# Kernel tuning notes

Measured on AMD Instinct MI355X. Metric: run time of the kernel, lower is better.

Reference implementation:

```python
import jax, jax.numpy as jnp
import numpy as np
import math

B, S, D = 1, 2048, 512
H = 8
DH = D // H
WIN = 128  # window_size
EPS = 1e-5


def _layernorm(x, g, b):
    mu = jnp.mean(x, axis=-1, keepdims=True)
    var = jnp.mean((x - mu) ** 2, axis=-1, keepdims=True)
    return (x - mu) * jax.lax.rsqrt(var + EPS) * g + b


def _local_attention(q, k, v, window_size):
    # q,k,v: [B,H,S,DH]. Faithful to F.pad + unfold: zero-padded keys
    # participate in softmax with score 0 (no masking), as in the original.
    w = window_size // 2
    W = 2 * w + 1
    kp = jnp.pad(k, ((0, 0), (0, 0), (w, w), (0, 0)))
    vp = jnp.pad(v, ((0, 0), (0, 0), (w, w), (0, 0)))
    idx = jnp.arange(q.shape[2])[:, None] + jnp.arange(W)[None, :]  # [S,W]
    k_win = kp[:, :, idx]  # [B,H,S,W,DH]
    v_win = vp[:, :, idx]  # [B,H,S,W,DH]
    scores = jnp.einsum('bhsd,bhswd->bhsw', q, k_win) / math.sqrt(q.shape[-1])
    attn = jax.nn.softmax(scores, axis=-1)
    return jnp.einsum('bhsw,bhswd->bhsd', attn, v_win)


def setup_inputs() -> dict:
    key = jax.random.key(0)
    ks = jax.random.split(key, 8)
    sc = 0.02
    return {
        'x': jax.random.normal(ks[0], (B, S, D), dtype=jnp.float32),
        'w_qkv': jax.random.normal(ks[1], (D, 3 * D), dtype=jnp.float32) * sc,
        'b_qkv': jnp.zeros((3 * D,), dtype=jnp.float32),
        'w_out': jax.random.normal(ks[2], (D, D), dtype=jnp.float32) * sc,
        'b_out': jnp.zeros((D,), dtype=jnp.float32),
        'ln_g': jnp.ones((D,), dtype=jnp.float32),
        'ln_b': jnp.zeros((D,), dtype=jnp.float32),
        'w1': jax.random.normal(ks[3], (D, 4 * D), dtype=jnp.float32) * sc,
        'b1': jnp.zeros((4 * D,), dtype=jnp.float32),
        'w2': jax.random.normal(ks[4], (4 * D, D), dtype=jnp.float32) * sc,
        'b2': jnp.zeros((D,), dtype=jnp.float32),
    }


def reference(x, w_qkv, b_qkv, w_out, b_out, ln_g, ln_b, w1, b1, w2, b2):
    residual = x
    xn = _layernorm(x, ln_g, ln_b)
    qkv = xn @ w_qkv + b_qkv                       # [B,S,3D]
    qkv = qkv.reshape(B, S, 3, H, DH)
    qkv = jnp.transpose(qkv, (2, 0, 3, 1, 4))      # [3,B,H,S,DH]
    q, k, v = qkv[0], qkv[1], qkv[2]
    attn_out = _local_attention(q, k, v, WIN)       # [B,H,S,DH]
    attn_out = jnp.transpose(attn_out, (0, 2, 1, 3)).reshape(B, S, D)
    attn_out = attn_out @ w_out + b_out
    out = residual + attn_out
    # FFN applied directly to `out` (no second norm in original)
    ffn = jax.nn.gelu(out @ w1 + b1, approximate=False) @ w2 + b2
    return out + ffn
```

## Files before the change

kernel.cpp:

```cpp
#include <hip/hip_runtime.h>
#include <math.h>

#define S_LEN 2048
#define DMODEL 512
#define NHEAD 8
#define DHEAD 64
#define LN_EPS 1e-5f

typedef __bf16 bf16;
typedef __bf16 bf16x8 __attribute__((ext_vector_type(8)));
typedef __bf16 bf16x4 __attribute__((ext_vector_type(4)));
typedef __bf16 bf16x2 __attribute__((ext_vector_type(2)));
typedef float f32x4 __attribute__((ext_vector_type(4)));

__device__ __forceinline__ float wave_reduce_sum(float x) {
#pragma unroll
  for (int off = 32; off > 0; off >>= 1) x += __shfl_xor(x, off);
  return x;
}

__global__ __launch_bounds__(256) void prep_kernel(
    const float* __restrict__ x, const float* __restrict__ ln_g,
    const float* __restrict__ ln_b, const float* __restrict__ w_qkv,
    const float* __restrict__ w_out, const float* __restrict__ w1,
    const float* __restrict__ w2, bf16* __restrict__ xn,
    bf16* __restrict__ wqkvT, bf16* __restrict__ woutT,
    bf16* __restrict__ w1T, bf16* __restrict__ w2T) {
  __shared__ float t[32][33];
  int b = blockIdx.x;
  const int tid = threadIdx.x;
  if (b < 2048) {
    const float2 v = ((const float2*)(x + (size_t)b * DMODEL))[tid];
    float s = v.x + v.y;
    float s2 = v.x * v.x + v.y * v.y;
    s = wave_reduce_sum(s);
    s2 = wave_reduce_sum(s2);
    __shared__ float red[2][4];
    const int wv = tid >> 6, ln = tid & 63;
    if (ln == 0) { red[0][wv] = s; red[1][wv] = s2; }
    __syncthreads();
    s = red[0][0] + red[0][1] + red[0][2] + red[0][3];
    s2 = red[1][0] + red[1][1] + red[1][2] + red[1][3];
    const float mu = s * (1.0f / DMODEL);
    const float var = s2 * (1.0f / DMODEL) - mu * mu;
    const float rs = rsqrtf(var + LN_EPS);
    const float2 gg = ((const float2*)ln_g)[tid];
    const float2 bb = ((const float2*)ln_b)[tid];
    bf16x2 o;
    o[0] = (bf16)((v.x - mu) * rs * gg.x + bb.x);
    o[1] = (bf16)((v.y - mu) * rs * gg.y + bb.y);
    ((bf16x2*)(xn + (size_t)b * DMODEL))[tid] = o;
    return;
  }
  b -= 2048;
  const float* W; bf16* WT; int K, N, bx, by;
  if (b < 768)       { W = w_qkv; WT = wqkvT; K = 512;  N = 1536; bx = b % 48; by = b / 48; }
  else if (b < 1024) { b -= 768;  W = w_out; WT = woutT; K = 512;  N = 512;  bx = b % 16; by = b / 16; }
  else if (b < 2048) { b -= 1024; W = w1;    WT = w1T;   K = 512;  N = 2048; bx = b % 64; by = b / 64; }
  else               { b -= 2048; W = w2;    WT = w2T;   K = 2048; N = 512;  bx = b % 16; by = b / 16; }
  const int c = tid & 31, r8 = tid >> 5;
  const int n0 = bx * 32, k0 = by * 32;
#pragma unroll
  for (int it = 0; it < 4; it++) {
    const int r = r8 + it * 8;
    t[r][c] = W[(size_t)(k0 + r) * N + n0 + c];
  }
  __syncthreads();
#pragma unroll
  for (int it = 0; it < 4; it++) {
    const int r = r8 + it * 8;
    WT[(size_t)(n0 + r) * K + k0 + c] = (bf16)t[c][r];
  }
}

template <int MODE, int SPLITK>
__global__ __launch_bounds__(256) void mmC_kernel(const bf16* __restrict__ A,
                                                  const bf16* __restrict__ BT,
                                                  const float* __restrict__ bias,
                                                  bf16* __restrict__ Cb,
                                                  bf16* __restrict__ vT,
                                                  float* __restrict__ outF,
                                                  int N, int K, int gx) {
  __shared__ bf16 As[2][64 * 64];
  __shared__ bf16 Bs[2][64 * 64];
  const int tid = threadIdx.x;
  int b = blockIdx.x;
  int kh = 0;
  if (SPLITK > 0) { kh = b & 1; b >>= 1; }
  const int wave = tid >> 6, lane = tid & 63;
  const int lr = lane & 15, kg = lane >> 4;
  const int wm = wave & 1, wn = wave >> 1;
  const int rowBase = (b / gx) * 64, colBase = (b % gx) * 64;
  const int ldk = (SPLITK > 0) ? 2 * SPLITK : K;
  const int kBase = kh * ((SPLITK > 0) ? SPLITK : 0);

  const bf16* aP[2]; const bf16* bP[2]; int off[2];
#pragma unroll
  for (int r = 0; r < 2; ++r) {
    const int c = wave * 2 + r;
    const int elem = c * 512 + lane * 8;
    const int s = elem >> 11, row = (elem >> 5) & 63, kp = elem & 31;
    aP[r] = A + (size_t)(rowBase + row) * ldk + kBase + s * 32 + kp;
    bP[r] = BT + (size_t)(colBase + row) * ldk + kBase + s * 32 + kp;
    off[r] = c * 512;
  }
  auto stage = [&](int kk, int buf) {
#pragma unroll
    for (int r = 0; r < 2; ++r) {
      __builtin_amdgcn_global_load_lds(
          (const __attribute__((address_space(1))) void*)(aP[r] + kk),
          (__attribute__((address_space(3))) void*)(&As[buf][off[r]]), 16, 0, 0);
      __builtin_amdgcn_global_load_lds(
          (const __attribute__((address_space(1))) void*)(bP[r] + kk),
          (__attribute__((address_space(3))) void*)(&Bs[buf][off[r]]), 16, 0, 0);
    }
  };

  f32x4 acc[2][2] = {};
  const int niter = K >> 6;
  stage(0, 0);
  for (int it = 0; it < niter; ++it) {
    const int cur = it & 1;
    __syncthreads();
    if (it + 1 < niter) stage((it + 1) << 6, cur ^ 1);
    const bf16* as = As[cur];
    const bf16* bs = Bs[cur];
#pragma unroll
    for (int s = 0; s < 2; ++s) {
      bf16x8 af[2], bfr[2];
#pragma unroll
      for (int i = 0; i < 2; ++i)
        af[i] = *(const bf16x8*)(as + s * 2048 + (wm * 32 + i * 16 + lr) * 32 + kg * 8);
#pragma unroll
      for (int j = 0; j < 2; ++j)
        bfr[j] = *(const bf16x8*)(bs + s * 2048 + (wn * 32 + j * 16 + lr) * 32 + kg * 8);
#pragma unroll
      for (int i = 0; i < 2; ++i)
#pragma unroll
        for (int j = 0; j < 2; ++j)
          acc[i][j] = __builtin_amdgcn_mfma_f32_16x16x32_bf16(af[i], bfr[j],
                                                              acc[i][j], 0, 0, 0);
    }
  }

  if (SPLITK > 0) {
#pragma unroll
    for (int j = 0; j < 2; ++j) {
      const int col = colBase + wn * 32 + j * 16 + lr;
      const float bs = (kh == 0) ? bias[col] : 0.0f;
#pragma unroll
      for (int i = 0; i < 2; ++i)
#pragma unroll
        for (int r = 0; r < 4; ++r) {
          const size_t row = rowBase + wm * 32 + i * 16 + kg * 4 + r;
          unsafeAtomicAdd(&outF[row * N + col], acc[i][j][r] + bs);
        }
    }
    return;
  }

  if (MODE == 4 && colBase >= 1024) {
#pragma unroll
    for (int j = 0; j < 2; ++j) {
      const int col = colBase + wn * 32 + j * 16 + lr;
      const float bs = bias[col];
      bf16* dst = vT + (size_t)(col - 1024) * S_LEN;
#pragma unroll
      for (int i = 0; i < 2; ++i) {
        bf16x4 p;
#pragma unroll
        for (int r = 0; r < 4; ++r) p[r] = (bf16)(acc[i][j][r] + bs);
        *(bf16x4*)(dst + rowBase + wm * 32 + i * 16 + kg * 4) = p;
      }
    }
    return;
  }

  __syncthreads();
  bf16* Cs = (bf16*)As;
#pragma unroll
  for (int j = 0; j < 2; ++j) {
    const int colL = wn * 32 + j * 16 + lr;
    const float bs = bias[colBase + colL];
#pragma unroll
    for (int i = 0; i < 2; ++i)
#pragma unroll
      for (int r = 0; r < 4; ++r) {
        const int rowL = wm * 32 + i * 16 + kg * 4 + r;
        float v = acc[i][j][r] + bs;
        if (MODE == 2) v = 0.5f * v * (1.0f + erff(v * 0.70710678118654752f));
        Cs[rowL * 64 + colL] = (bf16)v;
      }
  }
  __syncthreads();
  {
    const int rowOut = tid >> 2, colOut = (tid & 3) * 16;
    const bf16x8 v0 = *(const bf16x8*)&Cs[rowOut * 64 + colOut];
    const bf16x8 v1 = *(const bf16x8*)&Cs[rowOut * 64 + colOut + 8];
    bf16* dst = Cb + (size_t)(rowBase + rowOut) * N + colBase + colOut;
    *(bf16x8*)dst = v0;
    *(bf16x8*)(dst + 8) = v1;
  }
}

__global__ __launch_bounds__(256) void mmB_kernel(const bf16* __restrict__ A,
                                                  const bf16* __restrict__ BT,
                                                  const float* __restrict__ bias,
                                                  const float* __restrict__ res,
                                                  float* __restrict__ Cf,
                                                  bf16* __restrict__ Cb,
                                                  int N, int K) {
  __shared__ bf16 As[2][32 * 64];
  __shared__ bf16 Bs[2][64 * 64];
  const int tid = threadIdx.x;
  const int wave = tid >> 6, lane = tid & 63;
  const int lr = lane & 15, kg = lane >> 4;
  const int rowBase = blockIdx.y * 32, colBase = blockIdx.x * 64;

  const bf16* aP; const bf16* bP[2]; int aOff, bOff[2];
  {
    const int elem = wave * 512 + lane * 8;
    const int s = elem >> 10, row = (elem >> 5) & 31, kp = elem & 31;
    aP = A + (size_t)(rowBase + row) * K + s * 32 + kp;
    aOff = wave * 512;
  }
#pragma unroll
  for (int r = 0; r < 2; ++r) {
    const int c = wave * 2 + r;
    const int elem = c * 512 + lane * 8;
    const int s = elem >> 11, row = (elem >> 5) & 63, kp = elem & 31;
    bP[r] = BT + (size_t)(colBase + row) * K + s * 32 + kp;
    bOff[r] = c * 512;
  }
  auto stage = [&](int kk, int buf) {
    __builtin_amdgcn_global_load_lds(
        (const __attribute__((address_space(1))) void*)(aP + kk),
        (__attribute__((address_space(3))) void*)(&As[buf][aOff]), 16, 0, 0);
#pragma unroll
    for (int r = 0; r < 2; ++r)
      __builtin_amdgcn_global_load_lds(
          (const __attribute__((address_space(1))) void*)(bP[r] + kk),
          (__attribute__((address_space(3))) void*)(&Bs[buf][bOff[r]]), 16, 0, 0);
  };

  f32x4 acc[2] = {};
  const int niter = K >> 6;
  stage(0, 0);
  for (int it = 0; it < niter; ++it) {
    const int cur = it & 1;
    __syncthreads();
    if (it + 1 < niter) stage((it + 1) << 6, cur ^ 1);
    const bf16* as = As[cur];
    const bf16* bs = Bs[cur];
#pragma unroll
    for (int s = 0; s < 2; ++s) {
      bf16x8 af[2], bfr;
#pragma unroll
      for (int i = 0; i < 2; ++i)
        af[i] = *(const bf16x8*)(as + s * 1024 + (i * 16 + lr) * 32 + kg * 8);
      bfr = *(const bf16x8*)(bs + s * 2048 + (wave * 16 + lr) * 32 + kg * 8);
#pragma unroll
      for (int i = 0; i < 2; ++i)
        acc[i] = __builtin_amdgcn_mfma_f32_16x16x32_bf16(af[i], bfr, acc[i], 0, 0, 0);
    }
  }

  {
    const int col = colBase + wave * 16 + lr;
    const float bs = bias[col];
#pragma unroll
    for (int i = 0; i < 2; ++i)
#pragma unroll
      for (int r = 0; r < 4; ++r) {
        const size_t row = rowBase + i * 16 + kg * 4 + r;
        const float v = acc[i][r] + bs + res[row * N + col];
        Cf[row * N + col] = v;
        Cb[row * N + col] = (bf16)v;
      }
  }
}

__global__ __launch_bounds__(256) void attn_fused(const bf16* __restrict__ qkvb,
                                                  const bf16* __restrict__ vT,
                                                  bf16* __restrict__ attnb) {
  __shared__ bf16 Kl[192][72];
  __shared__ bf16 Vt[64][200];
  __shared__ bf16 Ql[64][72];

  const int tid = threadIdx.x;
  const int s0 = blockIdx.x * 64;
  const int hc = blockIdx.y * DHEAD;

  {
    const int row = tid >> 2, c0 = (tid & 3) * 16;
    const bf16* src = qkvb + (size_t)(s0 + row) * 1536 + hc + c0;
    *(bf16x8*)&Ql[row][c0] = *(const bf16x8*)src;
    *(bf16x8*)&Ql[row][c0 + 8] = *(const bf16x8*)(src + 8);
  }
#pragma unroll
  for (int it = 0; it < 3; it++) {
    const int row = it * 64 + (tid >> 2), c0 = (tid & 3) * 16;
    const int p = s0 - 64 + row;
    bf16x8 a, b;
    if (p >= 0 && p < S_LEN) {
      const bf16* src = qkvb + (size_t)p * 1536 + 512 + hc + c0;
      a = *(const bf16x8*)src;
      b = *(const bf16x8*)(src + 8);
    } else {
#pragma unroll
      for (int j = 0; j < 8; j++) { a[j] = (bf16)0.f; b[j] = (bf16)0.f; }
    }
    *(bf16x8*)&Kl[row][c0] = a;
    *(bf16x8*)&Kl[row][c0 + 8] = b;
  }
  {
    const int d = tid >> 2, r0 = (tid & 3) * 48;
    const bf16* src = vT + (size_t)(hc + d) * S_LEN;
#pragma unroll
    for (int i = 0; i < 6; i++) {
      const int p0 = s0 - 64 + r0 + i * 8;
      bf16x8 v;
      if (p0 >= 0 && p0 + 8 <= S_LEN) {
        v = *(const bf16x8*)(src + p0);
      } else {
#pragma unroll
        for (int j = 0; j < 8; j++) {
          const int p = p0 + j;
          v[j] = (p >= 0 && p < S_LEN) ? src[p] : (bf16)0.f;
        }
      }
      *(bf16x8*)&Vt[d][r0 + i * 8] = v;
    }
  }
  __syncthreads();

  const int wv = tid >> 6, lane = tid & 63;
  const int lr = lane & 15, kg = lane >> 4;

  f32x4 c[12] = {};
#pragma unroll
  for (int step = 0; step < 2; step++) {
    const bf16x8 qf = *(const bf16x8*)&Ql[wv * 16 + lr][step * 32 + kg * 8];
#pragma unroll
    for (int t = 0; t < 12; t++) {
      const bf16x8 kf = *(const bf16x8*)&Kl[t * 16 + lr][step * 32 + kg * 8];
      c[t] = __builtin_amdgcn_mfma_f32_16x16x32_bf16(qf, kf, c[t], 0, 0, 0);
    }
  }

  float e[12][4];
  float inv[4];
#pragma unroll
  for (int rr = 0; rr < 4; rr++) {
    const int q = wv * 16 + kg * 4 + rr;
    float m = -1e30f;
#pragma unroll
    for (int t = 0; t < 12; t++) {
      const int col = t * 16 + lr;
      if (col >= q && col <= q + 128) m = fmaxf(m, c[t][rr] * 0.125f);
    }
#pragma unroll
    for (int off = 1; off < 16; off <<= 1) m = fmaxf(m, __shfl_xor(m, off));
    float sum = 0.f;
#pragma unroll
    for (int t = 0; t < 12; t++) {
      const int col = t * 16 + lr;
      const bool valid = (col >= q) && (col <= q + 128);
      const float ev = valid ? __expf(c[t][rr] * 0.125f - m) : 0.f;
      e[t][rr] = ev;
      sum += ev;
    }
#pragma unroll
    for (int off = 1; off < 16; off <<= 1) sum += __shfl_xor(sum, off);
    inv[rr] = 1.f / sum;
  }

  __syncthreads();

  bf16* Pl = (bf16*)Kl + wv * (16 * 200);
#pragma unroll
  for (int rr = 0; rr < 4; rr++)
#pragma unroll
    for (int t = 0; t < 12; t++)
      Pl[(kg * 4 + rr) * 200 + t * 16 + lr] = (bf16)(e[t][rr] * inv[rr]);

  f32x4 o[4] = {};
#pragma unroll
  for (int step = 0; step < 6; step++) {
    const bf16x8 pf = *(const bf16x8*)&Pl[lr * 200 + step * 32 + kg * 8];
#pragma unroll
    for (int jt = 0; jt < 4; jt++) {
      const bf16x8 vf = *(const bf16x8*)&Vt[jt * 16 + lr][step * 32 + kg * 8];
      o[jt] = __builtin_amdgcn_mfma_f32_16x16x32_bf16(pf, vf, o[jt], 0, 0, 0);
    }
  }

#pragma unroll
  for (int jt = 0; jt < 4; jt++)
#pragma unroll
    for (int rr = 0; rr < 4; rr++) {
      const int q = wv * 16 + kg * 4 + rr;
      attnb[(size_t)(s0 + q) * DMODEL + hc + jt * 16 + lr] = (bf16)o[jt][rr];
    }
}

extern "C" void kernel_launch(void* const* d_in, const int* in_sizes, int n_in,
                              void* d_out, int out_size, void* d_ws, size_t ws_size,
                              hipStream_t stream) {
  const float* x     = (const float*)d_in[0];
  const float* w_qkv = (const float*)d_in[1];
  const float* b_qkv = (const float*)d_in[2];
  const float* w_out = (const float*)d_in[3];
  const float* b_out = (const float*)d_in[4];
  const float* ln_g  = (const float*)d_in[5];
  const float* ln_b  = (const float*)d_in[6];
  const float* w1    = (const float*)d_in[7];
  const float* b1    = (const float*)d_in[8];
  const float* w2    = (const float*)d_in[9];
  const float* b2    = (const float*)d_in[10];
  float* out = (float*)d_out;

  char* w = (char*)d_ws;
  const size_t MB = 1u << 20;
  bf16* xn    = (bf16*)(w + 0);
  bf16* attnb = (bf16*)(w + 0);
  bf16* qkvb  = (bf16*)(w + 2 * MB);
  bf16* outb  = (bf16*)(w + 2 * MB);
  bf16* vT    = (bf16*)(w + 8 * MB);
  bf16* h1    = (bf16*)(w + 10 * MB);
  bf16* wqkvT = (bf16*)(w + 18 * MB);
  bf16* woutT = (bf16*)(w + 19 * MB + 512 * 1024);
  bf16* w1T   = (bf16*)(w + 20 * MB);
  bf16* w2T   = (bf16*)(w + 22 * MB);

  prep_kernel<<<5120, 256, 0, stream>>>(x, ln_g, ln_b, w_qkv, w_out, w1, w2,
                                        xn, wqkvT, woutT, w1T, w2T);
  mmC_kernel<4, 0><<<768, 256, 0, stream>>>(xn, wqkvT, b_qkv, qkvb, vT,
                                            nullptr, 1536, 512, 24);
  attn_fused<<<dim3(32, 8), 256, 0, stream>>>(qkvb, vT, attnb);
  mmB_kernel<<<dim3(8, 64), 256, 0, stream>>>(attnb, woutT, b_out, x, out,
                                              outb, 512, 512);
  mmC_kernel<2, 0><<<1024, 256, 0, stream>>>(outb, w1T, b1, h1, nullptr,
                                             nullptr, 2048, 512, 32);
  mmC_kernel<2, 1024><<<512, 256, 0, stream>>>(h1, w2T, b2, nullptr, nullptr,
                                               out, 512, 1024, 8);
}
```

Measured before the change: 140.3 us.

## Merge all stages into one persistent cooperative kernel with grid syncs

Replaces the six separate kernel launches (prep, QKV GEMM, attention, out-proj, FFN1, FFN2) with a single persistent cooperative mega-kernel that loops over phases and separates them with grid-wide barriers. Work items in each phase are distributed with grid-stride loops over an occupancy-sized grid. It also pads the Q/K and V buffers (new leading dimensions, plus zero-filled halo regions written in phase 0) so attention can skip boundary checks. The aim is to remove launch gaps and tail effects between stages. In exchange it adds grid-sync cost, ties all phases to one register and LDS budget, and keeps a per-phase launch fallback in case the cooperative launch fails.

After: 479.0 us. 241% more time.

```diff
diff --git a/kernel.cpp b/kernel.cpp
--- a/kernel.cpp
+++ b/kernel.cpp
@@ -1,11 +1,11 @@
 #include <hip/hip_runtime.h>
+#include <hip/hip_cooperative_groups.h>
 #include <math.h>
 
 #define S_LEN 2048
-#define DMODEL 512
-#define NHEAD 8
-#define DHEAD 64
 #define LN_EPS 1e-5f
+#define QPLD 1536
+#define VTLD 2240
 
 typedef __bf16 bf16;
 typedef __bf16 bf16x8 __attribute__((ext_vector_type(8)));
@@ -13,245 +13,125 @@
 typedef __bf16 bf16x2 __attribute__((ext_vector_type(2)));
 typedef float f32x4 __attribute__((ext_vector_type(4)));
 
-__device__ __forceinline__ float wave_reduce_sum(float x) {
+struct MegaArgs {
+  const float *x, *ln_g, *ln_b, *w_qkv, *b_qkv, *w_out, *b_out, *w1, *b1, *w2, *b2;
+  bf16 *xn, *wqkvT, *woutT, *w1T, *w2T, *qkvp, *vTp, *attnb, *outb, *h1;
+  float* out;
+};
+
+__device__ __forceinline__ void gll16(const bf16* g, bf16* l) {
+  __builtin_amdgcn_global_load_lds(
+      (const __attribute__((address_space(1))) void*)g,
+      (__attribute__((address_space(3))) void*)l, 16, 0, 0);
+}
+
+__device__ __forceinline__ float wave_reduce_sum64(float x) {
 #pragma unroll
   for (int off = 32; off > 0; off >>= 1) x += __shfl_xor(x, off);
   return x;
 }
 
-__global__ __launch_bounds__(256) void prep_kernel(
-    const float* __restrict__ x, const float* __restrict__ ln_g,
-    const float* __restrict__ ln_b, const float* __restrict__ w_qkv,
-    const float* __restrict__ w_out, const float* __restrict__ w1,
-    const float* __restrict__ w2, bf16* __restrict__ xn,
-    bf16* __restrict__ wqkvT, bf16* __restrict__ woutT,
-    bf16* __restrict__ w1T, bf16* __restrict__ w2T) {
-  __shared__ float t[32][33];
-  int b = blockIdx.x;
-  const int tid = threadIdx.x;
-  if (b < 2048) {
-    const float2 v = ((const float2*)(x + (size_t)b * DMODEL))[tid];
-    float s = v.x + v.y;
-    float s2 = v.x * v.x + v.y * v.y;
-    s = wave_reduce_sum(s);
-    s2 = wave_reduce_sum(s2);
-    __shared__ float red[2][4];
-    const int wv = tid >> 6, ln = tid & 63;
-    if (ln == 0) { red[0][wv] = s; red[1][wv] = s2; }
-    __syncthreads();
-    s = red[0][0] + red[0][1] + red[0][2] + red[0][3];
-    s2 = red[1][0] + red[1][1] + red[1][2] + red[1][3];
-    const float mu = s * (1.0f / DMODEL);
-    const float var = s2 * (1.0f / DMODEL) - mu * mu;
-    const float rs = rsqrtf(var + LN_EPS);
-    const float2 gg = ((const float2*)ln_g)[tid];
-    const float2 bb = ((const float2*)ln_b)[tid];
-    bf16x2 o;
-    o[0] = (bf16)((v.x - mu) * rs * gg.x + bb.x);
-    o[1] = (bf16)((v.y - mu) * rs * gg.y + bb.y);
-    ((bf16x2*)(xn + (size_t)b * DMODEL))[tid] = o;
-    return;
-  }
-  b -= 2048;
-  const float* W; bf16* WT; int K, N, bx, by;
-  if (b < 768)       { W = w_qkv; WT = wqkvT; K = 512;  N = 1536; bx = b % 48; by = b / 48; }
-  else if (b < 1024) { b -= 768;  W = w_out; WT = woutT; K = 512;  N = 512;  bx = b % 16; by = b / 16; }
-  else if (b < 2048) { b -= 1024; W = w1;    WT = w1T;   K = 512;  N = 2048; bx = b % 64; by = b / 64; }
-  else               { b -= 2048; W = w2;    WT = w2T;   K = 2048; N = 512;  bx = b % 16; by = b / 16; }
+__device__ __forceinline__ void transpose_tile(const float* W, bf16* WT, int K,
+                                               int N, int bx, int by,
+                                               float (*t)[33], int tid) {
   const int c = tid & 31, r8 = tid >> 5;
   const int n0 = bx * 32, k0 = by * 32;
 #pragma unroll
-  for (int it = 0; it < 4; it++) {
-    const int r = r8 + it * 8;
-    t[r][c] = W[(size_t)(k0 + r) * N + n0 + c];
-  }
+  for (int it = 0; it < 4; it++)
+    t[r8 + it * 8][c] = W[(size_t)(k0 + r8 + it * 8) * N + n0 + c];
   __syncthreads();
 #pragma unroll
-  for (int it = 0; it < 4; it++) {
-    const int r = r8 + it * 8;
-    WT[(size_t)(n0 + r) * K + k0 + c] = (bf16)t[c][r];
-  }
-}
-
-template <int MODE, int SPLITK>
-__global__ __launch_bounds__(256) void mmC_kernel(const bf16* __restrict__ A,
-                                                  const bf16* __restrict__ BT,
-                                                  const float* __restrict__ bias,
-                                                  bf16* __restrict__ Cb,
-                                                  bf16* __restrict__ vT,
-                                                  float* __restrict__ outF,
-                                                  int N, int K, int gx) {
-  __shared__ bf16 As[2][64 * 64];
-  __shared__ bf16 Bs[2][64 * 64];
-  const int tid = threadIdx.x;
-  int b = blockIdx.x;
-  int kh = 0;
-  if (SPLITK > 0) { kh = b & 1; b >>= 1; }
+  for (int it = 0; it < 4; it++)
+    WT[(size_t)(n0 + r8 + it * 8) * K + k0 + c] = (bf16)t[c][r8 + it * 8];
+  __syncthreads();
+}
+
+__device__ __forceinline__ void mm64_kloop(const bf16* A, const bf16* BT,
+                                           int rowBase, int colBase, int tid,
+                                           char* smem, f32x4 (*acc)[2]) {
+  bf16* AsB = (bf16*)smem;
+  bf16* BsB = (bf16*)(smem + 16384);
   const int wave = tid >> 6, lane = tid & 63;
   const int lr = lane & 15, kg = lane >> 4;
   const int wm = wave & 1, wn = wave >> 1;
-  const int rowBase = (b / gx) * 64, colBase = (b % gx) * 64;
-  const int ldk = (SPLITK > 0) ? 2 * SPLITK : K;
-  const int kBase = kh * ((SPLITK > 0) ? SPLITK : 0);
-
   const bf16* aP[2]; const bf16* bP[2]; int off[2];
 #pragma unroll
   for (int r = 0; r < 2; ++r) {
     const int c = wave * 2 + r;
     const int elem = c * 512 + lane * 8;
     const int s = elem >> 11, row = (elem >> 5) & 63, kp = elem & 31;
-    aP[r] = A + (size_t)(rowBase + row) * ldk + kBase + s * 32 + kp;
-    bP[r] = BT + (size_t)(colBase + row) * ldk + kBase + s * 32 + kp;
+    aP[r] = A + (size_t)(rowBase + row) * 512 + s * 32 + kp;
+    bP[r] = BT + (size_t)(colBase + row) * 512 + s * 32 + kp;
     off[r] = c * 512;
   }
   auto stage = [&](int kk, int buf) {
 #pragma unroll
     for (int r = 0; r < 2; ++r) {
-      __builtin_amdgcn_global_load_lds(
-          (const __attribute__((address_space(1))) void*)(aP[r] + kk),
-          (__attribute__((address_space(3))) void*)(&As[buf][off[r]]), 16, 0, 0);
-      __builtin_amdgcn_global_load_lds(
-          (const __attribute__((address_space(1))) void*)(bP[r] + kk),
-          (__attribute__((address_space(3))) void*)(&Bs[buf][off[r]]), 16, 0, 0);
+      gll16(aP[r] + kk, AsB + buf * 4096 + off[r]);
+      gll16(bP[r] + kk, BsB + buf * 4096 + off[r]);
     }
   };
-
-  f32x4 acc[2][2] = {};
-  const int niter = K >> 6;
+  stage(0, 0);
+  for (int it = 0; it < 8; ++it) {
+    const int cur = it & 1;
+    __syncthreads();
+    if (it < 7) stage((it + 1) << 6, cur ^ 1);
+    const bf16* as = AsB + cur * 4096;
+    const bf16* bs = BsB + cur * 4096;
+#pragma unroll
+    for (int s = 0; s < 2; ++s) {
+      bf16x8 af[2], bfr[2];
+#pragma unroll
+      for (int i = 0; i < 2; ++i)
+        af[i] = *(const bf16x8*)(as + s * 2048 + (wm * 32 + i * 16 + lr) * 32 + kg * 8);
+#pragma unroll
+      for (int j = 0; j < 2; ++j)
+        bfr[j] = *(const bf16x8*)(bs + s * 2048 + (wn * 32 + j * 16 + lr) * 32 + kg * 8);
+#pragma unroll
+      for (int i = 0; i < 2; ++i)
+#pragma unroll
+        for (int j = 0; j < 2; ++j)
+          acc[i][j] = __builtin_amdgcn_mfma_f32_16x16x32_bf16(af[i], bfr[j],
+                                                              acc[i][j], 0, 0, 0);
+    }
+  }
+}
+
+__device__ __forceinline__ void mm32_kloop(const bf16* A, const bf16* BT,
+                                           int ldk, int kBase, int niter,
+                                           int rowBase, int colBase, int tid,
+                                           char* smem, f32x4* acc) {
+  bf16* AsB = (bf16*)smem;
+  bf16* BsB = (bf16*)(smem + 8192);
+  const int wave = tid >> 6, lane = tid & 63;
+  const int lr = lane & 15, kg = lane >> 4;
+  const bf16* aP; const bf16* bP[2]; int aOff, bOff[2];
+  {
+    const int elem = wave * 512 + lane * 8;
+    const int s = elem >> 10, row = (elem >> 5) & 31, kp = elem & 31;
+    aP = A + (size_t)(rowBase + row) * ldk + kBase + s * 32 + kp;
+    aOff = wave * 512;
+  }
+#pragma unroll
+  for (int r = 0; r < 2; ++r) {
+    const int c = wave * 2 + r;
+    const int elem = c * 512 + lane * 8;
+    const int s = elem >> 11, row = (elem >> 5) & 63, kp = elem & 31;
+    bP[r] = BT + (size_t)(colBase + row) * ldk + kBase + s * 32 + kp;
+    bOff[r] = c * 512;
+  }
+  auto stage = [&](int kk, int buf) {
+    gll16(aP + kk, AsB + buf * 2048 + aOff);
+#pragma unroll
+    for (int r = 0; r < 2; ++r) gll16(bP[r] + kk, BsB + buf * 4096 + bOff[r]);
+  };
   stage(0, 0);
   for (int it = 0; it < niter; ++it) {
     const int cur = it & 1;
     __syncthreads();
     if (it + 1 < niter) stage((it + 1) << 6, cur ^ 1);
-    const bf16* as = As[cur];
-    const bf16* bs = Bs[cur];
-#pragma unroll
-    for (int s = 0; s < 2; ++s) {
-      bf16x8 af[2], bfr[2];
-#pragma unroll
-      for (int i = 0; i < 2; ++i)
-        af[i] = *(const bf16x8*)(as + s * 2048 + (wm * 32 + i * 16 + lr) * 32 + kg * 8);
-#pragma unroll
-      for (int j = 0; j < 2; ++j)
-        bfr[j] = *(const bf16x8*)(bs + s * 2048 + (wn * 32 + j * 16 + lr) * 32 + kg * 8);
-#pragma unroll
-      for (int i = 0; i < 2; ++i)
-#pragma unroll
-        for (int j = 0; j < 2; ++j)
-          acc[i][j] = __builtin_amdgcn_mfma_f32_16x16x32_bf16(af[i], bfr[j],
-                                                              acc[i][j], 0, 0, 0);
-    }
-  }
-
-  if (SPLITK > 0) {
-#pragma unroll
-    for (int j = 0; j < 2; ++j) {
-      const int col = colBase + wn * 32 + j * 16 + lr;
-      const float bs = (kh == 0) ? bias[col] : 0.0f;
-#pragma unroll
-      for (int i = 0; i < 2; ++i)
-#pragma unroll
-        for (int r = 0; r < 4; ++r) {
-          const size_t row = rowBase + wm * 32 + i * 16 + kg * 4 + r;
-          unsafeAtomicAdd(&outF[row * N + col], acc[i][j][r] + bs);
-        }
-    }
-    return;
-  }
-
-  if (MODE == 4 && colBase >= 1024) {
-#pragma unroll
-    for (int j = 0; j < 2; ++j) {
-      const int col = colBase + wn * 32 + j * 16 + lr;
-      const float bs = bias[col];
-      bf16* dst = vT + (size_t)(col - 1024) * S_LEN;
-#pragma unroll
-      for (int i = 0; i < 2; ++i) {
-        bf16x4 p;
-#pragma unroll
-        for (int r = 0; r < 4; ++r) p[r] = (bf16)(acc[i][j][r] + bs);
-        *(bf16x4*)(dst + rowBase + wm * 32 + i * 16 + kg * 4) = p;
-      }
-    }
-    return;
-  }
-
-  __syncthreads();
-  bf16* Cs = (bf16*)As;
-#pragma unroll
-  for (int j = 0; j < 2; ++j) {
-    const int colL = wn * 32 + j * 16 + lr;
-    const float bs = bias[colBase + colL];
-#pragma unroll
-    for (int i = 0; i < 2; ++i)
-#pragma unroll
-      for (int r = 0; r < 4; ++r) {
-        const int rowL = wm * 32 + i * 16 + kg * 4 + r;
-        float v = acc[i][j][r] + bs;
-        if (MODE == 2) v = 0.5f * v * (1.0f + erff(v * 0.70710678118654752f));
-        Cs[rowL * 64 + colL] = (bf16)v;
-      }
-  }
-  __syncthreads();
-  {
-    const int rowOut = tid >> 2, colOut = (tid & 3) * 16;
-    const bf16x8 v0 = *(const bf16x8*)&Cs[rowOut * 64 + colOut];
-    const bf16x8 v1 = *(const bf16x8*)&Cs[rowOut * 64 + colOut + 8];
-    bf16* dst = Cb + (size_t)(rowBase + rowOut) * N + colBase + colOut;
-    *(bf16x8*)dst = v0;
-    *(bf16x8*)(dst + 8) = v1;
-  }
-}
-
-__global__ __launch_bounds__(256) void mmB_kernel(const bf16* __restrict__ A,
-                                                  const bf16* __restrict__ BT,
-                                                  const float* __restrict__ bias,
-                                                  const float* __restrict__ res,
-                                                  float* __restrict__ Cf,
-                                                  bf16* __restrict__ Cb,
-                                                  int N, int K) {
-  __shared__ bf16 As[2][32 * 64];
-  __shared__ bf16 Bs[2][64 * 64];
-  const int tid = threadIdx.x;
-  const int wave = tid >> 6, lane = tid & 63;
-  const int lr = lane & 15, kg = lane >> 4;
-  const int rowBase = blockIdx.y * 32, colBase = blockIdx.x * 64;
-
-  const bf16* aP; const bf16* bP[2]; int aOff, bOff[2];
-  {
-    const int elem = wave * 512 + lane * 8;
-    const int s = elem >> 10, row = (elem >> 5) & 31, kp = elem & 31;
-    aP = A + (size_t)(rowBase + row) * K + s * 32 + kp;
-    aOff = wave * 512;
-  }
-#pragma unroll
-  for (int r = 0; r < 2; ++r) {
-    const int c = wave * 2 + r;
-    const int elem = c * 512 + lane * 8;
-    const int s = elem >> 11, row = (elem >> 5) & 63, kp = elem & 31;
-    bP[r] = BT + (size_t)(colBase + row) * K + s * 32 + kp;
-    bOff[r] = c * 512;
-  }
-  auto stage = [&](int kk, int buf) {
-    __builtin_amdgcn_global_load_lds(
-        (const __attribute__((address_space(1))) void*)(aP + kk),
-        (__attribute__((address_space(3))) void*)(&As[buf][aOff]), 16, 0, 0);
-#pragma unroll
-    for (int r = 0; r < 2; ++r)
-      __builtin_amdgcn_global_load_lds(
-          (const __attribute__((address_space(1))) void*)(bP[r] + kk),
-          (__attribute__((address_space(3))) void*)(&Bs[buf][bOff[r]]), 16, 0, 0);
-  };
-
-  f32x4 acc[2] = {};
-  const int niter = K >> 6;
-  stage(0, 0);
-  for (int it = 0; it < niter; ++it) {
-    const int cur = it & 1;
-    __syncthreads();
-    if (it + 1 < niter) stage((it + 1) << 6, cur ^ 1);
-    const bf16* as = As[cur];
-    const bf16* bs = Bs[cur];
+    const bf16* as = AsB + cur * 2048;
+    const bf16* bs = BsB + cur * 4096;
 #pragma unroll
     for (int s = 0; s < 2; ++s) {
       bf16x8 af[2], bfr;
@@ -264,184 +144,301 @@
         acc[i] = __builtin_amdgcn_mfma_f32_16x16x32_bf16(af[i], bfr, acc[i], 0, 0, 0);
     }
   }
-
-  {
-    const int col = colBase + wave * 16 + lr;
-    const float bs = bias[col];
-#pragma unroll
-    for (int i = 0; i < 2; ++i)
-#pragma unroll
-      for (int r = 0; r < 4; ++r) {
-        const size_t row = rowBase + i * 16 + kg * 4 + r;
-        const float v = acc[i][r] + bs + res[row * N + col];
-        Cf[row * N + col] = v;
-        Cb[row * N + col] = (bf16)v;
-      }
-  }
-}
-
-__global__ __launch_bounds__(256) void attn_fused(const bf16* __restrict__ qkvb,
-                                                  const bf16* __restrict__ vT,
-                                                  bf16* __restrict__ attnb) {
-  __shared__ bf16 Kl[192][72];
-  __shared__ bf16 Vt[64][200];
-  __shared__ bf16 Ql[64][72];
-
+}
+
+__global__ __launch_bounds__(256, 4) void mega_kernel(MegaArgs a, int phaseLo,
+                                                      int phaseHi) {
+  __shared__ __align__(16) char smem[32768];
   const int tid = threadIdx.x;
-  const int s0 = blockIdx.x * 64;
-  const int hc = blockIdx.y * DHEAD;
-
-  {
-    const int row = tid >> 2, c0 = (tid & 3) * 16;
-    const bf16* src = qkvb + (size_t)(s0 + row) * 1536 + hc + c0;
-    *(bf16x8*)&Ql[row][c0] = *(const bf16x8*)src;
-    *(bf16x8*)&Ql[row][c0 + 8] = *(const bf16x8*)(src + 8);
-  }
-#pragma unroll
-  for (int it = 0; it < 3; it++) {
-    const int row = it * 64 + (tid >> 2), c0 = (tid & 3) * 16;
-    const int p = s0 - 64 + row;
-    bf16x8 a, b;
-    if (p >= 0 && p < S_LEN) {
-      const bf16* src = qkvb + (size_t)p * 1536 + 512 + hc + c0;
-      a = *(const bf16x8*)src;
-      b = *(const bf16x8*)(src + 8);
+
+  for (int ph = phaseLo; ph <= phaseHi; ++ph) {
+    if (ph > phaseLo) cooperative_groups::this_grid().sync();
+
+    if (ph == 0) {
+      float(*t)[33] = (float(*)[33])smem;
+      float* red = (float*)(smem + 8192);
+      for (int wk = blockIdx.x; wk < 5776; wk += gridDim.x) {
+        if (wk < 2048) {
+          const int row = wk;
+          const float2 v = ((const float2*)(a.x + (size_t)row * 512))[tid];
+          float s = wave_reduce_sum64(v.x + v.y);
+          float s2 = wave_reduce_sum64(v.x * v.x + v.y * v.y);
+          const int wv = tid >> 6, ln = tid & 63;
+          if (ln == 0) { red[wv] = s; red[4 + wv] = s2; }
+          __syncthreads();
+          s = red[0] + red[1] + red[2] + red[3];
+          s2 = red[4] + red[5] + red[6] + red[7];
+          const float mu = s * (1.0f / 512);
+          const float var = s2 * (1.0f / 512) - mu * mu;
+          const float rs = rsqrtf(var + LN_EPS);
+          const float2 gg = ((const float2*)a.ln_g)[tid];
+          const float2 bb = ((const float2*)a.ln_b)[tid];
+          bf16x2 o;
+          o[0] = (bf16)((v.x - mu) * rs * gg.x + bb.x);
+          o[1] = (bf16)((v.y - mu) * rs * gg.y + bb.y);
+          ((bf16x2*)(a.xn + (size_t)row * 512))[tid] = o;
+          __syncthreads();
+        } else if (wk < 5120) {
+          int b = wk - 2048;
+          if (b < 768)       transpose_tile(a.w_qkv, a.wqkvT, 512, 1536, b % 48, b / 48, t, tid);
+          else if (b < 1024) { b -= 768;  transpose_tile(a.w_out, a.woutT, 512, 512,  b % 16, b / 16, t, tid); }
+          else if (b < 2048) { b -= 1024; transpose_tile(a.w1,   a.w1T,   512, 2048, b % 64, b / 64, t, tid); }
+          else               { b -= 2048; transpose_tile(a.w2,   a.w2T,   2048, 512, b % 16, b / 16, t, tid); }
+        } else {
+          const int z = wk - 5120;
+          bf16* p;
+          if (z < 96) {
+            size_t base = (z < 48) ? (size_t)z * 2048
+                                   : (size_t)2112 * QPLD + (size_t)(z - 48) * 2048;
+            p = a.qkvp + base;
+          } else {
+            p = a.vTp + (size_t)(z - 96) * 2048;
+          }
+          bf16x8 zv;
+#pragma unroll
+          for (int j = 0; j < 8; j++) zv[j] = (bf16)0.f;
+          *(bf16x8*)(p + tid * 8) = zv;
+        }
+      }
+    } else if (ph == 1) {
+      for (int wk = blockIdx.x; wk < 768; wk += gridDim.x) {
+        const int rowBase = (wk / 24) * 64, colBase = (wk % 24) * 64;
+        const int wave = tid >> 6, lane = tid & 63;
+        const int lr = lane & 15, kg = lane >> 4;
+        const int wm = wave & 1, wn = wave >> 1;
+        f32x4 acc[2][2] = {};
+        mm64_kloop(a.xn, a.wqkvT, rowBase, colBase, tid, smem, acc);
+        if (colBase >= 1024) {
+#pragma unroll
+          for (int j = 0; j < 2; ++j) {
+            const int col = colBase + wn * 32 + j * 16 + lr;
+            const float bs = a.b_qkv[col];
+            bf16* dst = a.vTp + (size_t)(col - 1024) * VTLD + 64;
+#pragma unroll
+            for (int i = 0; i < 2; ++i) {
+              bf16x4 p;
+#pragma unroll
+              for (int r = 0; r < 4; ++r) p[r] = (bf16)(acc[i][j][r] + bs);
+              *(bf16x4*)(dst + rowBase + wm * 32 + i * 16 + kg * 4) = p;
+            }
+          }
+          __syncthreads();
+        } else {
+          __syncthreads();
+          bf16* Cs = (bf16*)smem;
+#pragma unroll
+          for (int j = 0; j < 2; ++j) {
+            const int colL = wn * 32 + j * 16 + lr;
+            const float bs = a.b_qkv[colBase + colL];
+#pragma unroll
+            for (int i = 0; i < 2; ++i)
+#pragma unroll
+              for (int r = 0; r < 4; ++r)
+                Cs[(wm * 32 + i * 16 + kg * 4 + r) * 64 + colL] =
+                    (bf16)(acc[i][j][r] + bs);
+          }
+          __syncthreads();
+          const int rowOut = tid >> 2, colOut = (tid & 3) * 16;
+          bf16* dst = a.qkvp + (size_t)(64 + rowBase + rowOut) * QPLD + colBase + colOut;
+          *(bf16x8*)dst = *(const bf16x8*)&Cs[rowOut * 64 + colOut];
+          *(bf16x8*)(dst + 8) = *(const bf16x8*)&Cs[rowOut * 64 + colOut + 8];
+          __syncthreads();
+        }
+      }
+    } else if (ph == 2) {
+      for (int wk = blockIdx.x; wk < 256; wk += gridDim.x) {
+        const int s0 = (wk & 31) * 64;
+        const int hc = (wk >> 5) * 64;
+        bf16* Kl = (bf16*)smem;
+        {
+          const int c0 = (tid & 3) * 16;
+#pragma unroll
+          for (int it = 0; it < 3; it++) {
+            const int row = it * 64 + (tid >> 2);
+            const bf16* src = a.qkvp + (size_t)(s0 + row) * QPLD + 512 + hc + c0;
+            *(bf16x8*)&Kl[row * 72 + c0] = *(const bf16x8*)src;
+            *(bf16x8*)&Kl[row * 72 + c0 + 8] = *(const bf16x8*)(src + 8);
+          }
+        }
+        __syncthreads();
+        const int wv = tid >> 6, lane = tid & 63;
+        const int lr = lane & 15, kg = lane >> 4;
+        f32x4 c[12] = {};
+#pragma unroll
+        for (int step = 0; step < 2; step++) {
+          const bf16x8 qf = *(const bf16x8*)(a.qkvp +
+              (size_t)(64 + s0 + wv * 16 + lr) * QPLD + hc + step * 32 + kg * 8);
+#pragma unroll
+          for (int t = 0; t < 12; t++) {
+            const bf16x8 kf = *(const bf16x8*)&Kl[(t * 16 + lr) * 72 + step * 32 + kg * 8];
+            c[t] = __builtin_amdgcn_mfma_f32_16x16x32_bf16(qf, kf, c[t], 0, 0, 0);
+          }
+        }
+        __syncthreads();
+        bf16* Pl = (bf16*)smem + wv * 3200;
+        float inv[4];
+#pragma unroll
+        for (int rr = 0; rr < 4; rr++) {
+          const int q = wv * 16 + kg * 4 + rr;
+          float m = -1e30f;
+#pragma unroll
+          for (int t = 0; t < 12; t++) {
+            const int col = t * 16 + lr;
+            if (col >= q && col <= q + 128) m = fmaxf(m, c[t][rr] * 0.125f);
+          }
+#pragma unroll
+          for (int off = 1; off < 16; off <<= 1) m = fmaxf(m, __shfl_xor(m, off));
+          float sum = 0.f;
+#pragma unroll
+          for (int t = 0; t < 12; t++) {
+            const int col = t * 16 + lr;
+            const bool valid = (col >= q) && (col <= q + 128);
+            const float ev = valid ? __expf(c[t][rr] * 0.125f - m) : 0.f;
+            sum += ev;
+            Pl[(kg * 4 + rr) * 200 + col] = (bf16)ev;
+          }
+#pragma unroll
+          for (int off = 1; off < 16; off <<= 1) sum += __shfl_xor(sum, off);
+          inv[rr] = 1.f / sum;
+        }
+        f32x4 o[4] = {};
+#pragma unroll
+        for (int step = 0; step < 6; step++) {
+          const bf16x8 pf = *(const bf16x8*)&Pl[lr * 200 + step * 32 + kg * 8];
+#pragma unroll
+          for (int jt = 0; jt < 4; jt++) {
+            const bf16x8 vf = *(const bf16x8*)(a.vTp +
+                (size_t)(hc + jt * 16 + lr) * VTLD + s0 + step * 32 + kg * 8);
+            o[jt] = __builtin_amdgcn_mfma_f32_16x16x32_bf16(pf, vf, o[jt], 0, 0, 0);
+          }
+        }
+#pragma unroll
+        for (int jt = 0; jt < 4; jt++)
+#pragma unroll
+          for (int rr = 0; rr < 4; rr++) {
+            const int q = wv * 16 + kg * 4 + rr;
+            a.attnb[(size_t)(s0 + q) * 512 + hc + jt * 16 + lr] =
+                (bf16)(o[jt][rr] * inv[rr]);
+          }
+        __syncthreads();
+      }
+    } else if (ph == 3) {
+      for (int wk = blockIdx.x; wk < 512; wk += gridDim.x) {
+        const int rowBase = (wk / 8) * 32, colBase = (wk % 8) * 64;
+        const int wave = tid >> 6, lane = tid & 63;
+        const int lr = lane & 15, kg = lane >> 4;
+        f32x4 acc[2] = {};
+        mm32_kloop(a.attnb, a.woutT, 512, 0, 8, rowBase, colBase, tid, smem, acc);
+        const int col = colBase + wave * 16 + lr;
+        const float bs = a.b_out[col];
+#pragma unroll
+        for (int i = 0; i < 2; ++i)
+#pragma unroll
+          for (int r = 0; r < 4; ++r) {
+            const size_t row = rowBase + i * 16 + kg * 4 + r;
+            const float v = acc[i][r] + bs + a.x[row * 512 + col];
+            a.out[row * 512 + col] = v;
+            a.outb[row * 512 + col] = (bf16)v;
+          }
+      }
+    } else if (ph == 4) {
+      for (int wk = blockIdx.x; wk < 1024; wk += gridDim.x) {
+        const int rowBase = (wk / 32) * 64, colBase = (wk % 32) * 64;
+        const int wave = tid >> 6, lane = tid & 63;
+        const int lr = lane & 15, kg = lane >> 4;
+        const int wm = wave & 1, wn = wave >> 1;
+        f32x4 acc[2][2] = {};
+        mm64_kloop(a.outb, a.w1T, rowBase, colBase, tid, smem, acc);
+        __syncthreads();
+        bf16* Cs = (bf16*)smem;
+#pragma unroll
+        for (int j = 0; j < 2; ++j) {
+          const int colL = wn * 32 + j * 16 + lr;
+          const float bs = a.b1[colBase + colL];
+#pragma unroll
+          for (int i = 0; i < 2; ++i)
+#pragma unroll
+            for (int r = 0; r < 4; ++r) {
+              float v = acc[i][j][r] + bs;
+              v = 0.5f * v * (1.0f + erff(v * 0.70710678118654752f));
+              Cs[(wm * 32 + i * 16 + kg * 4 + r) * 64 + colL] = (bf16)v;
+            }
+        }
+        __syncthreads();
+        const int rowOut = tid >> 2, colOut = (tid & 3) * 16;
+        bf16* dst = a.h1 + (size_t)(rowBase + rowOut) * 2048 + colBase + colOut;
+        *(bf16x8*)dst = *(const bf16x8*)&Cs[rowOut * 64 + colOut];
+        *(bf16x8*)(dst + 8) = *(const bf16x8*)&Cs[rowOut * 64 + colOut + 8];
+        __syncthreads();
+      }
     } else {
-#pragma unroll
-      for (int j = 0; j < 8; j++) { a[j] = (bf16)0.f; b[j] = (bf16)0.f; }
+      for (int wk = blockIdx.x; wk < 1024; wk += gridDim.x) {
+        const int kh = wk & 1, tile = wk >> 1;
+        const int rowBase = (tile >> 3) * 32, colBase = (tile & 7) * 64;
+        const int wave = tid >> 6, lane = tid & 63;
+        const int lr = lane & 15, kg = lane >> 4;
+        f32x4 acc[2] = {};
+        mm32_kloop(a.h1, a.w2T, 2048, kh * 1024, 16, rowBase, colBase, tid,
+                   smem, acc);
+        const int col = colBase + wave * 16 + lr;
+        const float bs = (kh == 0) ? a.b2[col] : 0.0f;
+#pragma unroll
+        for (int i = 0; i < 2; ++i)
+#pragma unroll
+          for (int r = 0; r < 4; ++r) {
+            const size_t row = rowBase + i * 16 + kg * 4 + r;
+            unsafeAtomicAdd(&a.out[row * 512 + col], acc[i][r] + bs);
+          }
+      }
     }
-    *(bf16x8*)&Kl[row][c0] = a;
-    *(bf16x8*)&Kl[row][c0 + 8] = b;
-  }
-  {
-    const int d = tid >> 2, r0 = (tid & 3) * 48;
-    const bf16* src = vT + (size_t)(hc + d) * S_LEN;
-#pragma unroll
-    for (int i = 0; i < 6; i++) {
-      const int p0 = s0 - 64 + r0 + i * 8;
-      bf16x8 v;
-      if (p0 >= 0 && p0 + 8 <= S_LEN) {
-        v = *(const bf16x8*)(src + p0);
-      } else {
-#pragma unroll
-        for (int j = 0; j < 8; j++) {
-          const int p = p0 + j;
-          v[j] = (p >= 0 && p < S_LEN) ? src[p] : (bf16)0.f;
-        }
-      }
-      *(bf16x8*)&Vt[d][r0 + i * 8] = v;
-    }
-  }
-  __syncthreads();
-
-  const int wv = tid >> 6, lane = tid & 63;
-  const int lr = lane & 15, kg = lane >> 4;
-
-  f32x4 c[12] = {};
-#pragma unroll
-  for (int step = 0; step < 2; step++) {
-    const bf16x8 qf = *(const bf16x8*)&Ql[wv * 16 + lr][step * 32 + kg * 8];
-#pragma unroll
-    for (int t = 0; t < 12; t++) {
-      const bf16x8 kf = *(const bf16x8*)&Kl[t * 16 + lr][step * 32 + kg * 8];
-      c[t] = __builtin_amdgcn_mfma_f32_16x16x32_bf16(qf, kf, c[t], 0, 0, 0);
-    }
-  }
-
-  float e[12][4];
-  float inv[4];
-#pragma unroll
-  for (int rr = 0; rr < 4; rr++) {
-    const int q = wv * 16 + kg * 4 + rr;
-    float m = -1e30f;
-#pragma unroll
-    for (int t = 0; t < 12; t++) {
-      const int col = t * 16 + lr;
-      if (col >= q && col <= q + 128) m = fmaxf(m, c[t][rr] * 0.125f);
-    }
-#pragma unroll
-    for (int off = 1; off < 16; off <<= 1) m = fmaxf(m, __shfl_xor(m, off));
-    float sum = 0.f;
-#pragma unroll
-    for (int t = 0; t < 12; t++) {
-      const int col = t * 16 + lr;
-      const bool valid = (col >= q) && (col <= q + 128);
-      const float ev = valid ? __expf(c[t][rr] * 0.125f - m) : 0.f;
-      e[t][rr] = ev;
-      sum += ev;
-    }
-#pragma unroll
-    for (int off = 1; off < 16; off <<= 1) sum += __shfl_xor(sum, off);
-    inv[rr] = 1.f / sum;
-  }
-
-  __syncthreads();
-
-  bf16* Pl = (bf16*)Kl + wv * (16 * 200);
-#pragma unroll
-  for (int rr = 0; rr < 4; rr++)
-#pragma unroll
-    for (int t = 0; t < 12; t++)
-      Pl[(kg * 4 + rr) * 200 + t * 16 + lr] = (bf16)(e[t][rr] * inv[rr]);
-
-  f32x4 o[4] = {};
-#pragma unroll
-  for (int step = 0; step < 6; step++) {
-    const bf16x8 pf = *(const bf16x8*)&Pl[lr * 200 + step * 32 + kg * 8];
-#pragma unroll
-    for (int jt = 0; jt < 4; jt++) {
-      const bf16x8 vf = *(const bf16x8*)&Vt[jt * 16 + lr][step * 32 + kg * 8];
-      o[jt] = __builtin_amdgcn_mfma_f32_16x16x32_bf16(pf, vf, o[jt], 0, 0, 0);
-    }
-  }
-
-#pragma unroll
-  for (int jt = 0; jt < 4; jt++)
-#pragma unroll
-    for (int rr = 0; rr < 4; rr++) {
-      const int q = wv * 16 + kg * 4 + rr;
-      attnb[(size_t)(s0 + q) * DMODEL + hc + jt * 16 + lr] = (bf16)o[jt][rr];
-    }
+  }
 }
 
 extern "C" void kernel_launch(void* const* d_in, const int* in_sizes, int n_in,
                               void* d_out, int out_size, void* d_ws, size_t ws_size,
                               hipStream_t stream) {
-  const float* x     = (const float*)d_in[0];
-  const float* w_qkv = (const float*)d_in[1];
-  const float* b_qkv = (const float*)d_in[2];
-  const float* w_out = (const float*)d_in[3];
-  const float* b_out = (const float*)d_in[4];
-  const float* ln_g  = (const float*)d_in[5];
-  const float* ln_b  = (const float*)d_in[6];
-  const float* w1    = (const float*)d_in[7];
-  const float* b1    = (const float*)d_in[8];
-  const float* w2    = (const float*)d_in[9];
-  const float* b2    = (const float*)d_in[10];
-  float* out = (float*)d_out;
-
   char* w = (char*)d_ws;
   const size_t MB = 1u << 20;
-  bf16* xn    = (bf16*)(w + 0);
-  bf16* attnb = (bf16*)(w + 0);
-  bf16* qkvb  = (bf16*)(w + 2 * MB);
-  bf16* outb  = (bf16*)(w + 2 * MB);
-  bf16* vT    = (bf16*)(w + 8 * MB);
-  bf16* h1    = (bf16*)(w + 10 * MB);
-  bf16* wqkvT = (bf16*)(w + 18 * MB);
-  bf16* woutT = (bf16*)(w + 19 * MB + 512 * 1024);
-  bf16* w1T   = (bf16*)(w + 20 * MB);
-  bf16* w2T   = (bf16*)(w + 22 * MB);
-
-  prep_kernel<<<5120, 256, 0, stream>>>(x, ln_g, ln_b, w_qkv, w_out, w1, w2,
-                                        xn, wqkvT, woutT, w1T, w2T);
-  mmC_kernel<4, 0><<<768, 256, 0, stream>>>(xn, wqkvT, b_qkv, qkvb, vT,
-                                            nullptr, 1536, 512, 24);
-  attn_fused<<<dim3(32, 8), 256, 0, stream>>>(qkvb, vT, attnb);
-  mmB_kernel<<<dim3(8, 64), 256, 0, stream>>>(attnb, woutT, b_out, x, out,
-                                              outb, 512, 512);
-  mmC_kernel<2, 0><<<1024, 256, 0, stream>>>(outb, w1T, b1, h1, nullptr,
-                                             nullptr, 2048, 512, 32);
-  mmC_kernel<2, 1024><<<512, 256, 0, stream>>>(h1, w2T, b2, nullptr, nullptr,
-                                               out, 512, 1024, 8);
-}
+  MegaArgs a;
+  a.x = (const float*)d_in[0];
+  a.w_qkv = (const float*)d_in[1];
+  a.b_qkv = (const float*)d_in[2];
+  a.w_out = (const float*)d_in[3];
+  a.b_out = (const float*)d_in[4];
+  a.ln_g = (const float*)d_in[5];
+  a.ln_b = (const float*)d_in[6];
+  a.w1 = (const float*)d_in[7];
+  a.b1 = (const float*)d_in[8];
+  a.w2 = (const float*)d_in[9];
+  a.b2 = (const float*)d_in[10];
+  a.out = (float*)d_out;
+  a.xn    = (bf16*)(w + 0);
+  a.attnb = (bf16*)(w + 0);
+  a.qkvp  = (bf16*)(w + 2 * MB);
+  a.outb  = (bf16*)(w + 2 * MB);
+  a.vTp   = (bf16*)(w + 9 * MB);
+  a.h1    = (bf16*)(w + 12 * MB);
+  a.wqkvT = (bf16*)(w + 20 * MB);
+  a.woutT = (bf16*)(w + 22 * MB);
+  a.w1T   = (bf16*)(w + 23 * MB);
+  a.w2T   = (bf16*)(w + 25 * MB);
+
+  int maxB = 0;
+  hipError_t oe =
+      hipOccupancyMaxActiveBlocksPerMultiprocessor(&maxB, mega_kernel, 256, 0);
+  int grid = 1024;
+  if (oe == hipSuccess && maxB > 0 && maxB * 256 < grid) grid = maxB * 256;
+
+  int lo = 0, hi = 5;
+  void* args[] = {(void*)&a, (void*)&lo, (void*)&hi};
+  hipError_t err = hipLaunchCooperativeKernel((const void*)mega_kernel,
+                                              dim3(grid), dim3(256), args, 0,
+                                              stream);
+  if (err != hipSuccess) {
+    (void)hipGetLastError();
+    const int pg[6] = {5776, 768, 256, 512, 1024, 1024};
+    for (int ph = 0; ph < 6; ++ph)
+      hipLaunchKernelGGL(mega_kernel, dim3(pg[ph]), dim3(256), 0, stream, a,
+                         ph, ph);
+  }
+}
```
